# Kernel optimization log

Measured on AMD Instinct MI355X. Metric: run time of the kernel, lower is better.

## Reference

```python
import jax, jax.numpy as jnp
import numpy as np
from jax import lax

IN_CHANNELS = 192
KERNEL_SIZES = (3, 5, 7)
SPLITS = (64, 64, 64)  # _split_channels(192, 3)


def _depthwise(x, w, k):
    # x: [N, c, H, W], w: [c, 1, k, k] (torch OIHW, groups=c, bias=False)
    pad = (k - 1) // 2
    c = x.shape[1]
    return lax.conv_general_dilated(
        x, w,
        window_strides=(1, 1),
        padding=[(pad, pad), (pad, pad)],
        feature_group_count=c,
        dimension_numbers=('NCHW', 'OIHW', 'NCHW'),
    )


def setup_inputs() -> dict:
    key = jax.random.key(0)
    kx, k3, k5, k7 = jax.random.split(key, 4)
    x = jax.random.normal(kx, (32, IN_CHANNELS, 112, 112), dtype=jnp.float32)
    w3 = jax.random.normal(k3, (SPLITS[0], 1, 3, 3), dtype=jnp.float32) * 0.1
    w5 = jax.random.normal(k5, (SPLITS[1], 1, 5, 5), dtype=jnp.float32) * 0.1
    w7 = jax.random.normal(k7, (SPLITS[2], 1, 7, 7), dtype=jnp.float32) * 0.1
    return {"x": x, "w3": w3, "w5": w5, "w7": w7}


def reference(x, w3, w5, w7):
    # torch.split along channel dim into SPLITS, per-group depthwise conv, concat
    boundaries = np.cumsum(SPLITS)[:-1].tolist()  # [64, 128]
    x1, x2, x3 = jnp.split(x, boundaries, axis=1)
    o1 = _depthwise(x1, w3, 3)
    o2 = _depthwise(x2, w5, 5)
    o3 = _depthwise(x3, w7, 7)
    return jnp.concatenate([o1, o2, o3], axis=1)
```

## Files before the change

kernel.cpp:

```cpp
#include <hip/hip_runtime.h>


#define HW 112
#define TILE_H 16
#define QROW 28
#define LQ 30
#define LSTRIDE (LQ * 16)
#define NR_MAX (TILE_H + 6)
#define C_TOTAL 192
#define N_BATCH 32

typedef float f4 __attribute__((ext_vector_type(4)));

template <int K>
__device__ __forceinline__ void conv_tile(const float* __restrict__ x,
                                          const float* __restrict__ w,
                                          float* __restrict__ out, char* lds,
                                          int cglob, int wc, int n, int tile0) {
  constexpr int PAD = (K - 1) / 2;
  constexpr int NR = TILE_H + K - 1;
  constexpr int TOT = NR * QROW;
  constexpr int SITERS = (TOT + 255) / 256;
  constexpr int CTOT = TILE_H * QROW;

  const int tid = threadIdx.x;
  const size_t plane = ((size_t)n * C_TOTAL + cglob) * (HW * HW);
  const float* xp = x + plane;

  float wr[K * K];
#pragma unroll
  for (int i = 0; i < K * K; ++i) wr[i] = w[wc * K * K + i];

  const f4 z4 = {0.f, 0.f, 0.f, 0.f};
  f4 sv[SITERS];
#pragma unroll
  for (int it = 0; it < SITERS; ++it) {
    const int unit = tid + it * 256;
    const int row = unit / QROW;
    const int cu = unit - row * QROW;
    const int ih = tile0 - PAD + row;
    const bool ok = (unit < TOT) && (ih >= 0) && (ih < HW);
    const int ihc = (ih < 0) ? 0 : ((ih > HW - 1) ? HW - 1 : ih);
    const f4 t = *(const f4*)(xp + (size_t)ihc * HW + cu * 4);
    sv[it] = ok ? t : z4;
  }
#pragma unroll
  for (int it = 0; it < SITERS; ++it) {
    const int unit = tid + it * 256;
    const int row = unit / QROW;
    const int cu = unit - row * QROW;
    if (unit < TOT) *(f4*)(lds + row * LSTRIDE + 16 + cu * 16) = sv[it];
  }
  if (tid < NR) *(f4*)(lds + tid * LSTRIDE) = z4;
  if (tid >= 128 && tid < 128 + NR)
    *(f4*)(lds + (tid - 128) * LSTRIDE + (LQ - 1) * 16) = z4;
  __syncthreads();

  char* const outb = (char*)(out + plane + (size_t)tile0 * HW);
#pragma unroll
  for (int b = 0; b < 2; ++b) {
    const int unit = tid + b * 256;
    if (unit < CTOT) {
      const int row = unit / QROW;
      const int q = unit - row * QROW;
      const char* base = lds + row * LSTRIDE + q * 16;

      float acc[4] = {0.f, 0.f, 0.f, 0.f};
#pragma unroll
      for (int r = 0; r < K; ++r) {
        const char* rb = base + r * LSTRIDE;
        const f4 L = *(const f4*)(rb);
        const f4 M = *(const f4*)(rb + 16);
        const f4 R = *(const f4*)(rb + 32);
        const float buf[12] = {L.x, L.y, L.z, L.w, M.x, M.y,
                               M.z, M.w, R.x, R.y, R.z, R.w};
#pragma unroll
        for (int dx = 0; dx < K; ++dx) {
          const float wt = wr[r * K + dx];
#pragma unroll
          for (int j = 0; j < 4; ++j)
            acc[j] = fmaf(wt, buf[4 + j + dx - PAD], acc[j]);
        }
      }
      f4 v = {acc[0], acc[1], acc[2], acc[3]};
      __builtin_nontemporal_store(v, (f4*)(outb + (size_t)unit * 16));
    }
  }
}

__global__ __launch_bounds__(256) void mixconv_lds(
    const float* __restrict__ x, const float* __restrict__ w3,
    const float* __restrict__ w5, const float* __restrict__ w7,
    float* __restrict__ out) {
  __shared__ __align__(16) char lds[NR_MAX * LSTRIDE];
  const int cy = blockIdx.y;
  const int n = blockIdx.z;
  const int tile0 = blockIdx.x * TILE_H;
  if (cy < 64)
    conv_tile<3>(x, w3, out, lds, cy, cy, n, tile0);
  else if (cy < 128)
    conv_tile<5>(x, w5, out, lds, cy, cy - 64, n, tile0);
  else
    conv_tile<7>(x, w7, out, lds, cy, cy - 128, n, tile0);
}

extern "C" void kernel_launch(void* const* d_in, const int* in_sizes, int n_in,
                              void* d_out, int out_size, void* d_ws,
                              size_t ws_size, hipStream_t stream) {
  const float* x = (const float*)d_in[0];
  const float* w3 = (const float*)d_in[1];
  const float* w5 = (const float*)d_in[2];
  const float* w7 = (const float*)d_in[3];
  float* out = (float*)d_out;

  const dim3 grid(HW / TILE_H, C_TOTAL, N_BATCH);
  const dim3 block(256);
  mixconv_lds<<<grid, block, 0, stream>>>(x, w3, w5, w7, out);
}
```

Measured before the change: 117.7 us.

## Compute two output rows per thread and enlarge row tile to 28

Each thread now produces two vertically adjacent output rows, so every LDS row it loads feeds both accumulators. This cuts LDS reads per output from K to roughly (K+1)/2. The row tile grows from 16 to 28, which reduces halo overhead and the block count. The LDS row stride changes to 496 bytes, and the larger tile raises LDS use and register pressure, which may lower occupancy.

```diff
diff --git a/kernel.cpp b/kernel.cpp
--- a/kernel.cpp
+++ b/kernel.cpp
@@ -2,10 +2,9 @@
 
 
 #define HW 112
-#define TILE_H 16
+#define TILE_H 28
 #define QROW 28
-#define LQ 30
-#define LSTRIDE (LQ * 16)
+#define LSTRIDE 496
 #define NR_MAX (TILE_H + 6)
 #define C_TOTAL 192
 #define N_BATCH 32
@@ -21,7 +20,7 @@
   constexpr int NR = TILE_H + K - 1;
   constexpr int TOT = NR * QROW;
   constexpr int SITERS = (TOT + 255) / 256;
-  constexpr int CTOT = TILE_H * QROW;
+  constexpr int CTOT = (TILE_H / 2) * QROW;
 
   const int tid = threadIdx.x;
   const size_t plane = ((size_t)n * C_TOTAL + cglob) * (HW * HW);
@@ -53,7 +52,7 @@
   }
   if (tid < NR) *(f4*)(lds + tid * LSTRIDE) = z4;
   if (tid >= 128 && tid < 128 + NR)
-    *(f4*)(lds + (tid - 128) * LSTRIDE + (LQ - 1) * 16) = z4;
+    *(f4*)(lds + (tid - 128) * LSTRIDE + 29 * 16) = z4;
   __syncthreads();
 
   char* const outb = (char*)(out + plane + (size_t)tile0 * HW);
@@ -61,13 +60,13 @@
   for (int b = 0; b < 2; ++b) {
     const int unit = tid + b * 256;
     if (unit < CTOT) {
-      const int row = unit / QROW;
-      const int q = unit - row * QROW;
-      const char* base = lds + row * LSTRIDE + q * 16;
+      const int rp = unit / QROW;
+      const int q = unit - rp * QROW;
+      const char* base = lds + rp * 2 * LSTRIDE + q * 16;
 
-      float acc[4] = {0.f, 0.f, 0.f, 0.f};
+      float acc[2][4] = {{0.f, 0.f, 0.f, 0.f}, {0.f, 0.f, 0.f, 0.f}};
 #pragma unroll
-      for (int r = 0; r < K; ++r) {
+      for (int r = 0; r < K + 1; ++r) {
         const char* rb = base + r * LSTRIDE;
         const f4 L = *(const f4*)(rb);
         const f4 M = *(const f4*)(rb + 16);
@@ -75,15 +74,24 @@
         const float buf[12] = {L.x, L.y, L.z, L.w, M.x, M.y,
                                M.z, M.w, R.x, R.y, R.z, R.w};
 #pragma unroll
-        for (int dx = 0; dx < K; ++dx) {
-          const float wt = wr[r * K + dx];
+        for (int o = 0; o < 2; ++o) {
+          const int dy = r - o;
+          if (dy >= 0 && dy < K) {
 #pragma unroll
-          for (int j = 0; j < 4; ++j)
-            acc[j] = fmaf(wt, buf[4 + j + dx - PAD], acc[j]);
+            for (int dx = 0; dx < K; ++dx) {
+              const float wt = wr[dy * K + dx];
+#pragma unroll
+              for (int j = 0; j < 4; ++j)
+                acc[o][j] = fmaf(wt, buf[4 + j + dx - PAD], acc[o][j]);
+            }
+          }
         }
       }
-      f4 v = {acc[0], acc[1], acc[2], acc[3]};
-      __builtin_nontemporal_store(v, (f4*)(outb + (size_t)unit * 16));
+      char* const o0 = outb + (size_t)(rp * 2) * (HW * 4) + q * 16;
+      f4 v0 = {acc[0][0], acc[0][1], acc[0][2], acc[0][3]};
+      f4 v1 = {acc[1][0], acc[1][1], acc[1][2], acc[1][3]};
+      __builtin_nontemporal_store(v0, (f4*)(o0));
+      __builtin_nontemporal_store(v1, (f4*)(o0 + HW * 4));
     }
   }
 }
```

Measured after the change: 109.1 us, median of 2. 7.3% less time.
